# Performance work log

Hardware: AMD Instinct MI355X
Metric: run time of the kernel (lower is better)

## Reference

```python
import jax, jax.numpy as jnp
import numpy as np

MAX_DISP = 4  # max_displacement
PAD = MAX_DISP
ODIM = 2 * MAX_DISP + 1  # 9 -> 81 cost-volume channels


def setup_inputs() -> dict:
    key = jax.random.key(0)
    k1, k2 = jax.random.split(key)
    B, C, H, W = 4, 256, 96, 192
    x1 = jax.random.normal(k1, (B, C, H, W), dtype=jnp.float32)
    x2 = jax.random.normal(k2, (B, C, H, W), dtype=jnp.float32)
    return {"x1": x1, "x2": x2}


def reference(x1, x2):
    B, C, H, W = x1.shape
    # zero-pad x2 spatially by PAD on each side (matches F.pad([pad]*4))
    x2p = jnp.pad(x2, ((0, 0), (0, 0), (PAD, PAD), (PAD, PAD)))
    cv = []
    for i in range(ODIM):          # fixed 9x9 displacement grid
        for j in range(ODIM):
            shifted = jax.lax.dynamic_slice(
                x2p, (0, 0, i, j), (B, C, H, W))
            # mean over channel dim -> [B, H, W]
            cv.append(jnp.mean(x1 * shifted, axis=1))
    return jnp.stack(cv, axis=1)  # [B, 81, H, W]
```

## Files before the change

### kernel.cpp

```cpp
#include <hip/hip_runtime.h>
#include <stddef.h>


#define NB 4
#define NC 256
#define HH 96
#define WW 192
#define TW 16
#define TH 4
#define KC 32
#define CHW (HH * WW)

#define HP 104
#define WP 208
#define PROW (WP * NC)
#define PIMG (HP * PROW)
#define XT2_ELEMS (NB * PIMG)
#define XT2_BYTES ((size_t)XT2_ELEMS * 2)

typedef __attribute__((ext_vector_type(8))) short bf16x8;
typedef __attribute__((ext_vector_type(4))) float f32x4;

__device__ __forceinline__ unsigned short f2bf(float f) {
    union { float f; unsigned u; } c; c.f = f;
    unsigned r = c.u + 0x7FFFu + ((c.u >> 16) & 1u);
    return (unsigned short)(r >> 16);
}

#define NTOP (NB * 8 * WP * 32)
#define NSIDE (NB * HH * 16 * 32)
__global__ __launch_bounds__(256) void pad_zero(unsigned short* __restrict__ xt2p)
{
    const uint4 z = make_uint4(0, 0, 0, 0);
    int t = blockIdx.x * 256 + threadIdx.x;
    const int stride = gridDim.x * 256;
    for (; t < NTOP + NSIDE; t += stride) {
        unsigned e;
        if (t < NTOP) {
            const int cg = t & 31;
            const int w  = (t >> 5) % WP;
            const int rr = (t >> 5) / WP;
            const int b  = rr >> 3;
            const int hh = rr & 7;
            const int hp = hh < 4 ? hh : 96 + hh;
            e = (unsigned)((b * HP + hp) * WP + w) * NC + cg * 8;
        } else {
            const int u  = t - NTOP;
            const int cg = u & 31;
            const int ws = (u >> 5) & 15;
            const int rr = (u >> 5) >> 4;
            const int b  = rr / HH;
            const int hp = 4 + rr % HH;
            const int wp = ws < 4 ? ws : 192 + ws;
            e = (unsigned)((b * HP + hp) * WP + wp) * NC + cg * 8;
        }
        *(uint4*)&xt2p[e] = z;
    }
}

__global__ __launch_bounds__(256) void transpose_x2(
    const float* __restrict__ x2, unsigned short* __restrict__ xt2p)
{
    __shared__ float t[64][65];
    int lin = blockIdx.x;
    const int wt = lin % 3; lin /= 3;
    const int ct = lin & 3; lin >>= 2;
    const int h  = lin % 96; lin /= 96;
    const int b  = lin & 3;
    const int w0 = wt * 64, c0 = ct * 64;

    const int wi = threadIdx.x & 63, c4 = threadIdx.x >> 6;
#pragma unroll
    for (int it = 0; it < 16; ++it) {
        const int c = it * 4 + c4;
        t[c][wi] = x2[((size_t)((b * NC + c0 + c) * HH + h)) * WW + w0 + wi];
    }
    __syncthreads();
#pragma unroll
    for (int it = 0; it < 2; ++it) {
        const int task = it * 256 + threadIdx.x;
        const int cg = task & 7;
        const int w  = task >> 3;
        bf16x8 v;
#pragma unroll
        for (int j = 0; j < 8; ++j) v[j] = (short)f2bf(t[cg * 8 + j][w]);
        const unsigned e = (unsigned)((b * HP + h + 4) * WP + (w0 + 4 + w)) * NC
                         + c0 + cg * 8;
        *(bf16x8*)&xt2p[e] = v;
    }
}

__global__ __launch_bounds__(512, 2) void corr_mfma_g(
    const float* __restrict__ x1,
    const unsigned short* __restrict__ xt2p,
    float* __restrict__ out)
{
    __shared__ float band[TH][9][9][18];

    const int lin = blockIdx.x;
    const int sw  = (lin & 7) * 144 + (lin >> 3);
    const int b   = sw / 288;
    const int t2  = sw - b * 288;
    const int ty  = t2 / 12;
    const int tx  = t2 - ty * 12;

    const int tid  = threadIdx.x;
    const int wv   = tid >> 6;
    const int lane = tid & 63;
    const int col  = lane & 15;
    const int q    = lane >> 4;
    const int r    = wv & 3;
    const int dig  = wv >> 2;
    const int w0   = tx * TW;
    const int h0   = ty * TH;
    const int h    = h0 + r;

    f32x4 acc[9];
#pragma unroll
    for (int s = 0; s < 9; ++s) acc[s] = (f32x4)0.0f;

    unsigned l2[9];
#pragma unroll
    for (int s = 0; s < 9; ++s) {
        const int u    = dig * 9 + s;
        const int di   = u >> 1;
        const int n    = (u & 1) * 16 + col;
        l2[s] = (unsigned)((b * HP + h + di) * WP + (w0 + n)) * NC + q * 8;
    }
    unsigned o1 = (unsigned)((b * NC + q * 8) * HH + h) * WW + w0 + col;

    float pa[8];
#pragma unroll
    for (int j = 0; j < 8; ++j) pa[j] = x1[o1 + j * CHW];
    o1 += KC * CHW;

    for (int ci = 0; ci < 8; ++ci) {
        bf16x8 bfr[9];
#pragma unroll
        for (int s = 0; s < 9; ++s) {
            bfr[s] = *(const bf16x8*)&xt2p[l2[s]];
            l2[s] += KC;
        }
        bf16x8 a;
#pragma unroll
        for (int j = 0; j < 8; ++j) a[j] = (short)f2bf(pa[j]);
        if (ci < 7) {
#pragma unroll
            for (int j = 0; j < 8; ++j) pa[j] = x1[o1 + j * CHW];
            o1 += KC * CHW;
        }
#pragma unroll
        for (int s = 0; s < 9; ++s)
            acc[s] = __builtin_amdgcn_mfma_f32_16x16x32_bf16(a, bfr[s], acc[s], 0, 0, 0);
    }

#pragma unroll
    for (int s = 0; s < 9; ++s) {
        const int u  = dig * 9 + s;
        const int di = u >> 1;
        const int uh = u & 1;
#pragma unroll
        for (int rg = 0; rg < 4; ++rg) {
            int m  = q * 4 + rg;
            int dj = uh * 16 + col - m;
            if (dj >= 0 && dj < 9)
                band[r][di][dj][m] = acc[s][rg];
        }
    }
    __syncthreads();

    const float scale = 1.0f / 256.0f;
#pragma unroll
    for (int it = 0; it < 11; ++it) {
        int gi = it * 32 + (tid >> 4);
        if (gi < 324) {
            int combo = gi >> 2;
            int row   = gi & 3;
            float v = band[row][combo / 9][combo % 9][tid & 15];
            out[((size_t)((b * 81 + combo) * HH + h0 + row)) * WW + w0 + (tid & 15)] = v * scale;
        }
    }
}

#define NROWS 12
#define NTASK 1152
#define KS 264
#define RS 1096
#define KSTRIDE (KC * CHW)
#define XBI(row, kg, n) ((row) * RS + (kg) * KS + (n) * 8)

__global__ __launch_bounds__(512, 4) void corr_mfma_fb(
    const float* __restrict__ x1, const float* __restrict__ x2,
    float* __restrict__ out)
{
    __shared__ union {
        unsigned short xb[NROWS * RS];
        float band[TH][9][9][18];
    } lds;

    const int lin = blockIdx.x;
    const int sw  = (lin & 7) * 144 + (lin >> 3);
    const int b   = sw / 288;
    const int t2  = sw - b * 288;
    const int ty  = t2 / 12;
    const int tx  = t2 - ty * 12;

    const int tid  = threadIdx.x;
    const int wv   = tid >> 6;
    const int lane = tid & 63;
    const int col  = lane & 15;
    const int q    = lane >> 4;
    const int r    = wv & 3;
    const int dig  = wv >> 2;
    const int w0   = tx * TW;
    const int h0   = ty * TH;
    const int h    = h0 + r;

    f32x4 acc[9];
#pragma unroll
    for (int s = 0; s < 9; ++s) acc[s] = (f32x4)0.0f;

    unsigned o2k[3];
    int      lofk[3];
    bool     okk[3];
    bool     act[3];
#pragma unroll
    for (int k = 0; k < 3; ++k) {
        const int t   = tid + k * 512;
        act[k] = (t < NTASK);
        const int seg = t % 6;
        const int u   = t / 6;
        const int cp  = u & 15;
        const int row = u >> 4;
        const int gh  = h0 - 4 + row;
        const int gw  = w0 - 4 + seg * 4;
        okk[k] = act[k] & (gh >= 0) & (gh < HH) & (gw >= 0) & (gw <= WW - 4);
        const int ghc = gh < 0 ? 0 : (gh > HH - 1 ? HH - 1 : gh);
        const int gwc = gw < 0 ? 0 : gw;
        const int rwc = row > NROWS - 1 ? NROWS - 1 : row;
        o2k[k]  = (unsigned)(((b * NC + cp * 2) * HH + ghc) * WW + gwc);
        lofk[k] = XBI(rwc, cp >> 2, seg * 4) + (cp & 3) * 2;
    }
    unsigned o1 = (unsigned)(((b * NC + q * 8) * HH + h) * WW + w0 + col);

    float pf[24];
    float pa[8];

#define STAGE_LOAD_FB()                                                  \
    {                                                                    \
        _Pragma("unroll")                                                \
        for (int k = 0; k < 3; ++k) {                                    \
            _Pragma("unroll")                                            \
            for (int e = 0; e < 2; ++e) {                                \
                float4 ld = make_float4(0.f, 0.f, 0.f, 0.f);             \
                if (okk[k]) ld = *(const float4*)&x2[o2k[k] + e * CHW];  \
                *(float4*)&pf[(k * 2 + e) * 4] = ld;                     \
            }                                                            \
            o2k[k] += KSTRIDE;                                           \
        }                                                                \
    }

#define X1_LOAD_FB()                                                     \
    {                                                                    \
        _Pragma("unroll")                                                \
        for (int j = 0; j < 8; ++j) pa[j] = x1[o1 + j * CHW];            \
        o1 += KSTRIDE;                                                   \
    }

    STAGE_LOAD_FB();
    X1_LOAD_FB();

    const int rbase = XBI(r, q, col);

    for (int ci = 0; ci < 8; ++ci) {
#pragma unroll
        for (int k = 0; k < 3; ++k) {
            if (act[k]) {
#pragma unroll
                for (int p = 0; p < 4; ++p) {
                    ushort2 v;
                    v.x = f2bf(pf[(k * 2 + 0) * 4 + p]);
                    v.y = f2bf(pf[(k * 2 + 1) * 4 + p]);
                    *(ushort2*)&lds.xb[lofk[k] + p * 8] = v;
                }
            }
        }
        __syncthreads();

        bf16x8 a;
#pragma unroll
        for (int j = 0; j < 8; ++j) a[j] = (short)f2bf(pa[j]);
        if (ci < 7) {
            STAGE_LOAD_FB();
            X1_LOAD_FB();
        }

#pragma unroll
        for (int s = 0; s < 9; ++s) {
            const int u    = dig * 9 + s;
            const int di   = u >> 1;
            const int half = u & 1;
            bf16x8 bb = *(const bf16x8*)&lds.xb[rbase + di * RS + half * 128];
            acc[s] = __builtin_amdgcn_mfma_f32_16x16x32_bf16(a, bb, acc[s], 0, 0, 0);
        }
        __syncthreads();
    }

#pragma unroll
    for (int s = 0; s < 9; ++s) {
        const int u  = dig * 9 + s;
        const int di = u >> 1;
        const int uh = u & 1;
#pragma unroll
        for (int rg = 0; rg < 4; ++rg) {
            int m  = q * 4 + rg;
            int dj = uh * 16 + col - m;
            if (dj >= 0 && dj < 9)
                lds.band[r][di][dj][m] = acc[s][rg];
        }
    }
    __syncthreads();

    const float scale = 1.0f / 256.0f;
#pragma unroll
    for (int it = 0; it < 11; ++it) {
        int gi = it * 32 + (tid >> 4);
        if (gi < 324) {
            int combo = gi >> 2;
            int row   = gi & 3;
            float v = lds.band[row][combo / 9][combo % 9][tid & 15];
            out[((size_t)((b * 81 + combo) * HH + h0 + row)) * WW + w0 + (tid & 15)] = v * scale;
        }
    }
}

extern "C" void kernel_launch(void* const* d_in, const int* in_sizes, int n_in,
                              void* d_out, int out_size, void* d_ws, size_t ws_size,
                              hipStream_t stream) {
    const float* x1 = (const float*)d_in[0];
    const float* x2 = (const float*)d_in[1];
    float* out = (float*)d_out;

    if (ws_size >= XT2_BYTES) {
        unsigned short* xt2p = (unsigned short*)d_ws;
        pad_zero<<<dim3(512), 256, 0, stream>>>(xt2p);
        transpose_x2<<<dim3(4608), 256, 0, stream>>>(x2, xt2p);
        corr_mfma_g<<<dim3(1152), 512, 0, stream>>>(x1, xt2p, out);
    } else {
        corr_mfma_fb<<<dim3(1152), 512, 0, stream>>>(x1, x2, out);
    }
}
```

Baseline: 264.7 us.

## Pack x2 into MFMA-fragment tiles and double-buffer loads in smaller correlation blocks

Replaces the zero-pad and transpose kernels with one pack kernel. It writes padded x2 directly in per-wave MFMA B-fragment order, 1 KB contiguous tiles of 16 columns by 32 channels, so each lane's load is one contiguous 16-byte read. The correlation kernel now uses 256-thread blocks covering 2 rows instead of 4, runs at 3 blocks per CU, unrolls the channel loop and double-buffers the B-fragment loads. This cuts one launch and should make the main kernel's loads fully coalesced, at the cost of more blocks, more registers and more redundant x2 halo reads.

```diff
diff --git a/kernel.cpp b/kernel.cpp
--- a/kernel.cpp
+++ b/kernel.cpp
@@ -7,16 +7,16 @@
 #define HH 96
 #define WW 192
 #define TW 16
-#define TH 4
+#define TH 2
 #define KC 32
 #define CHW (HH * WW)
 
 #define HP 104
-#define WP 208
-#define PROW (WP * NC)
-#define PIMG (HP * PROW)
-#define XT2_ELEMS (NB * PIMG)
-#define XT2_BYTES ((size_t)XT2_ELEMS * 2)
+#define WT 13
+#define NCG 8
+#define TILE_US 512
+#define NTILES (NB * HP * WT * NCG)
+#define XT2_BYTES ((size_t)NTILES * 1024)
 
 typedef __attribute__((ext_vector_type(8))) short bf16x8;
 typedef __attribute__((ext_vector_type(4))) float f32x4;
@@ -27,75 +27,155 @@
     return (unsigned short)(r >> 16);
 }
 
-#define NTOP (NB * 8 * WP * 32)
-#define NSIDE (NB * HH * 16 * 32)
-__global__ __launch_bounds__(256) void pad_zero(unsigned short* __restrict__ xt2p)
+__global__ __launch_bounds__(256) void pack_x2(
+    const float* __restrict__ x2, unsigned short* __restrict__ ft)
 {
-    const uint4 z = make_uint4(0, 0, 0, 0);
-    int t = blockIdx.x * 256 + threadIdx.x;
-    const int stride = gridDim.x * 256;
-    for (; t < NTOP + NSIDE; t += stride) {
-        unsigned e;
-        if (t < NTOP) {
-            const int cg = t & 31;
-            const int w  = (t >> 5) % WP;
-            const int rr = (t >> 5) / WP;
-            const int b  = rr >> 3;
-            const int hh = rr & 7;
-            const int hp = hh < 4 ? hh : 96 + hh;
-            e = (unsigned)((b * HP + hp) * WP + w) * NC + cg * 8;
-        } else {
-            const int u  = t - NTOP;
-            const int cg = u & 31;
-            const int ws = (u >> 5) & 15;
-            const int rr = (u >> 5) >> 4;
-            const int b  = rr / HH;
-            const int hp = 4 + rr % HH;
-            const int wp = ws < 4 ? ws : 192 + ws;
-            e = (unsigned)((b * HP + hp) * WP + wp) * NC + cg * 8;
-        }
-        *(uint4*)&xt2p[e] = z;
-    }
-}
-
-__global__ __launch_bounds__(256) void transpose_x2(
-    const float* __restrict__ x2, unsigned short* __restrict__ xt2p)
-{
-    __shared__ float t[64][65];
-    int lin = blockIdx.x;
-    const int wt = lin % 3; lin /= 3;
-    const int ct = lin & 3; lin >>= 2;
-    const int h  = lin % 96; lin /= 96;
-    const int b  = lin & 3;
-    const int w0 = wt * 64, c0 = ct * 64;
-
-    const int wi = threadIdx.x & 63, c4 = threadIdx.x >> 6;
-#pragma unroll
-    for (int it = 0; it < 16; ++it) {
-        const int c = it * 4 + c4;
-        t[c][wi] = x2[((size_t)((b * NC + c0 + c) * HH + h)) * WW + w0 + wi];
-    }
-    __syncthreads();
-#pragma unroll
-    for (int it = 0; it < 2; ++it) {
-        const int task = it * 256 + threadIdx.x;
-        const int cg = task & 7;
-        const int w  = task >> 3;
-        bf16x8 v;
-#pragma unroll
-        for (int j = 0; j < 8; ++j) v[j] = (short)f2bf(t[cg * 8 + j][w]);
-        const unsigned e = (unsigned)((b * HP + h + 4) * WP + (w0 + 4 + w)) * NC
-                         + c0 + cg * 8;
-        *(bf16x8*)&xt2p[e] = v;
-    }
-}
-
-__global__ __launch_bounds__(512, 2) void corr_mfma_g(
+    const int wv   = threadIdx.x >> 6;
+    const int lane = threadIdx.x & 63;
+    const int col  = lane & 15;
+    const int q    = lane >> 4;
+
+    const int tid0 = blockIdx.x * 4 + wv;
+    int t = tid0;
+    const int cg = t & 7;  t >>= 3;
+    const int wt = t % WT; t /= WT;
+    const int hp = t % HP;
+    const int b  = t / HP;
+
+    const int gh = hp - 4;
+    const int gw = wt * 16 + col - 4;
+    const bool ok = (gh >= 0) & (gh < HH) & (gw >= 0) & (gw < WW);
+
+    bf16x8 v;
+    if (ok) {
+        const float* src = &x2[(unsigned)((b * NC + cg * 32 + q * 8) * HH + gh) * WW + gw];
+#pragma unroll
+        for (int j = 0; j < 8; ++j) v[j] = (short)f2bf(src[(size_t)j * CHW]);
+    } else {
+#pragma unroll
+        for (int j = 0; j < 8; ++j) v[j] = 0;
+    }
+    *(bf16x8*)&ft[(unsigned)tid0 * TILE_US + lane * 8] = v;
+}
+
+__global__ __launch_bounds__(256, 3) void corr_mfma_ft(
     const float* __restrict__ x1,
-    const unsigned short* __restrict__ xt2p,
+    const unsigned short* __restrict__ ft,
     float* __restrict__ out)
 {
     __shared__ float band[TH][9][9][18];
+
+    const int lin = blockIdx.x;
+    const int sw  = (lin & 7) * 288 + (lin >> 3);
+    const int b   = sw / 576;
+    const int rem = sw - b * 576;
+    const int ty  = rem / 12;
+    const int tx  = rem - ty * 12;
+
+    const int tid  = threadIdx.x;
+    const int wv   = tid >> 6;
+    const int lane = tid & 63;
+    const int col  = lane & 15;
+    const int q    = lane >> 4;
+    const int r    = wv >> 1;
+    const int dig  = wv & 1;
+    const int w0   = tx * TW;
+    const int h0   = ty * TH;
+    const int h    = h0 + r;
+
+    f32x4 acc[9];
+#pragma unroll
+    for (int s = 0; s < 9; ++s) acc[s] = (f32x4)0.0f;
+
+    unsigned l2[9];
+#pragma unroll
+    for (int s = 0; s < 9; ++s) {
+        const int u  = dig * 9 + s;
+        const int di = u >> 1;
+        const int uh = u & 1;
+        const unsigned tile = (unsigned)(((b * HP + h + di) * WT + (tx + uh)) * NCG);
+        l2[s] = tile * TILE_US + lane * 8;
+    }
+    unsigned o1 = (unsigned)((b * NC + q * 8) * HH + h) * WW + w0 + col;
+
+    bf16x8 bfr[2][9];
+#pragma unroll
+    for (int s = 0; s < 9; ++s) {
+        bfr[0][s] = *(const bf16x8*)&ft[l2[s]];
+        l2[s] += TILE_US;
+    }
+    float pa[8];
+#pragma unroll
+    for (int j = 0; j < 8; ++j) pa[j] = x1[o1 + j * CHW];
+    o1 += KC * CHW;
+
+#pragma unroll
+    for (int ci = 0; ci < 8; ++ci) {
+        const int cur = ci & 1;
+        const int nxt = cur ^ 1;
+        if (ci < 7) {
+#pragma unroll
+            for (int s = 0; s < 9; ++s) {
+                bfr[nxt][s] = *(const bf16x8*)&ft[l2[s]];
+                l2[s] += TILE_US;
+            }
+        }
+        bf16x8 a;
+#pragma unroll
+        for (int j = 0; j < 8; ++j) a[j] = (short)f2bf(pa[j]);
+        if (ci < 7) {
+#pragma unroll
+            for (int j = 0; j < 8; ++j) pa[j] = x1[o1 + j * CHW];
+            o1 += KC * CHW;
+        }
+#pragma unroll
+        for (int s = 0; s < 9; ++s)
+            acc[s] = __builtin_amdgcn_mfma_f32_16x16x32_bf16(a, bfr[cur][s], acc[s], 0, 0, 0);
+    }
+
+#pragma unroll
+    for (int s = 0; s < 9; ++s) {
+        const int u  = dig * 9 + s;
+        const int di = u >> 1;
+        const int uh = u & 1;
+#pragma unroll
+        for (int rg = 0; rg < 4; ++rg) {
+            int m  = q * 4 + rg;
+            int dj = uh * 16 + col - m;
+            if (dj >= 0 && dj < 9)
+                band[r][di][dj][m] = acc[s][rg];
+        }
+    }
+    __syncthreads();
+
+    const float scale = 1.0f / 256.0f;
+#pragma unroll
+    for (int it = 0; it < 11; ++it) {
+        int gi = it * 16 + (tid >> 4);
+        if (gi < 162) {
+            int combo = gi >> 1;
+            int row   = gi & 1;
+            float v = band[row][combo / 9][combo % 9][tid & 15];
+            out[((size_t)((b * 81 + combo) * HH + h0 + row)) * WW + w0 + (tid & 15)] = v * scale;
+        }
+    }
+}
+
+#define NROWS 12
+#define NTASK 1152
+#define KS 264
+#define RS 1096
+#define KSTRIDE (KC * CHW)
+#define XBI(row, kg, n) ((row) * RS + (kg) * KS + (n) * 8)
+
+__global__ __launch_bounds__(512, 4) void corr_mfma_fb(
+    const float* __restrict__ x1, const float* __restrict__ x2,
+    float* __restrict__ out)
+{
+    __shared__ union {
+        unsigned short xb[NROWS * RS];
+        float band[4][9][9][18];
+    } lds;
 
     const int lin = blockIdx.x;
     const int sw  = (lin & 7) * 144 + (lin >> 3);
@@ -112,108 +192,7 @@
     const int r    = wv & 3;
     const int dig  = wv >> 2;
     const int w0   = tx * TW;
-    const int h0   = ty * TH;
-    const int h    = h0 + r;
-
-    f32x4 acc[9];
-#pragma unroll
-    for (int s = 0; s < 9; ++s) acc[s] = (f32x4)0.0f;
-
-    unsigned l2[9];
-#pragma unroll
-    for (int s = 0; s < 9; ++s) {
-        const int u    = dig * 9 + s;
-        const int di   = u >> 1;
-        const int n    = (u & 1) * 16 + col;
-        l2[s] = (unsigned)((b * HP + h + di) * WP + (w0 + n)) * NC + q * 8;
-    }
-    unsigned o1 = (unsigned)((b * NC + q * 8) * HH + h) * WW + w0 + col;
-
-    float pa[8];
-#pragma unroll
-    for (int j = 0; j < 8; ++j) pa[j] = x1[o1 + j * CHW];
-    o1 += KC * CHW;
-
-    for (int ci = 0; ci < 8; ++ci) {
-        bf16x8 bfr[9];
-#pragma unroll
-        for (int s = 0; s < 9; ++s) {
-            bfr[s] = *(const bf16x8*)&xt2p[l2[s]];
-            l2[s] += KC;
-        }
-        bf16x8 a;
-#pragma unroll
-        for (int j = 0; j < 8; ++j) a[j] = (short)f2bf(pa[j]);
-        if (ci < 7) {
-#pragma unroll
-            for (int j = 0; j < 8; ++j) pa[j] = x1[o1 + j * CHW];
-            o1 += KC * CHW;
-        }
-#pragma unroll
-        for (int s = 0; s < 9; ++s)
-            acc[s] = __builtin_amdgcn_mfma_f32_16x16x32_bf16(a, bfr[s], acc[s], 0, 0, 0);
-    }
-
-#pragma unroll
-    for (int s = 0; s < 9; ++s) {
-        const int u  = dig * 9 + s;
-        const int di = u >> 1;
-        const int uh = u & 1;
-#pragma unroll
-        for (int rg = 0; rg < 4; ++rg) {
-            int m  = q * 4 + rg;
-            int dj = uh * 16 + col - m;
-            if (dj >= 0 && dj < 9)
-                band[r][di][dj][m] = acc[s][rg];
-        }
-    }
-    __syncthreads();
-
-    const float scale = 1.0f / 256.0f;
-#pragma unroll
-    for (int it = 0; it < 11; ++it) {
-        int gi = it * 32 + (tid >> 4);
-        if (gi < 324) {
-            int combo = gi >> 2;
-            int row   = gi & 3;
-            float v = band[row][combo / 9][combo % 9][tid & 15];
-            out[((size_t)((b * 81 + combo) * HH + h0 + row)) * WW + w0 + (tid & 15)] = v * scale;
-        }
-    }
-}
-
-#define NROWS 12
-#define NTASK 1152
-#define KS 264
-#define RS 1096
-#define KSTRIDE (KC * CHW)
-#define XBI(row, kg, n) ((row) * RS + (kg) * KS + (n) * 8)
-
-__global__ __launch_bounds__(512, 4) void corr_mfma_fb(
-    const float* __restrict__ x1, const float* __restrict__ x2,
-    float* __restrict__ out)
-{
-    __shared__ union {
-        unsigned short xb[NROWS * RS];
-        float band[TH][9][9][18];
-    } lds;
-
-    const int lin = blockIdx.x;
-    const int sw  = (lin & 7) * 144 + (lin >> 3);
-    const int b   = sw / 288;
-    const int t2  = sw - b * 288;
-    const int ty  = t2 / 12;
-    const int tx  = t2 - ty * 12;
-
-    const int tid  = threadIdx.x;
-    const int wv   = tid >> 6;
-    const int lane = tid & 63;
-    const int col  = lane & 15;
-    const int q    = lane >> 4;
-    const int r    = wv & 3;
-    const int dig  = wv >> 2;
-    const int w0   = tx * TW;
-    const int h0   = ty * TH;
+    const int h0   = ty * 4;
     const int h    = h0 + r;
 
     f32x4 acc[9];
@@ -342,10 +321,9 @@
     float* out = (float*)d_out;
 
     if (ws_size >= XT2_BYTES) {
-        unsigned short* xt2p = (unsigned short*)d_ws;
-        pad_zero<<<dim3(512), 256, 0, stream>>>(xt2p);
-        transpose_x2<<<dim3(4608), 256, 0, stream>>>(x2, xt2p);
-        corr_mfma_g<<<dim3(1152), 512, 0, stream>>>(x1, xt2p, out);
+        unsigned short* ft = (unsigned short*)d_ws;
+        pack_x2<<<dim3(NTILES / 4), 256, 0, stream>>>(x2, ft);
+        corr_mfma_ft<<<dim3(2304), 256, 0, stream>>>(x1, ft, out);
     } else {
         corr_mfma_fb<<<dim3(1152), 512, 0, stream>>>(x1, x2, out);
     }
```

Result: faster. 250.4 us (-5.4%).
